# Kernel tuning notes

Hardware: AMD Instinct MI355X
Metric: run time of the kernel (lower is better)

The kernel has to match this reference:

```python
import jax, jax.numpy as jnp
import numpy as np


def setup_inputs() -> dict:
    key = jax.random.key(0)
    ks = jax.random.split(key, 8)
    N, NL, C, E, P3, P2, P1 = 2048, 16, 128, 10, 23, 4, 1
    return {
        "x": jax.random.normal(ks[0], (N, NL, C), dtype=jnp.float32),
        "atom_types": jax.random.randint(ks[1], (N,), 0, E),
        "U3": jax.random.normal(ks[2], (NL, NL, NL, P3), dtype=jnp.float32),
        "U2": jax.random.normal(ks[3], (NL, NL, P2), dtype=jnp.float32),
        "U1": jax.random.normal(ks[4], (NL, P1), dtype=jnp.float32),
        "W3": jax.random.normal(ks[5], (E, P3, C), dtype=jnp.float32),
        "W2": jax.random.normal(ks[6], (E, P2, C), dtype=jnp.float32),
        "W1": jax.random.normal(ks[7], (E, P1, C), dtype=jnp.float32),
    }


def reference(x, atom_types, U3, U2, U1, W3, W2, W1):
    # MACE symmetric contraction, correlation order 3, per-atom-type weights.
    # x: [N, nl, C]; atom_types: [N]; U3: [nl,nl,nl,P3]; W3: [E,P3,C]; etc.
    w3 = W3[atom_types]  # [N, P3, C]
    w2 = W2[atom_types]  # [N, P2, C]
    w1 = W1[atom_types]  # [N, P1, C]
    # Correlation-3 term: c3[n,a,b,c] = sum_{i,k} U3[a,b,i,k] * w3[n,k,c] * x[n,i,c]
    xw = jnp.einsum('nkc,nic->nkic', w3, x)        # [N, P3, nl, C]
    c3 = jnp.einsum('abik,nkic->nabc', U3, xw)     # [N, nl, nl, C]
    # Add correlation-2 term, contract one nl index with x.
    c2 = c3 + jnp.einsum('abk,nkc->nabc', U2, w2)  # [N, nl, nl, C]
    c1 = jnp.einsum('nabc,nbc->nac', c2, x)        # [N, nl, C]
    # Add correlation-1 term, contract last nl index with x.
    c1 = c1 + jnp.einsum('ak,nkc->nac', U1, w1)    # [N, nl, C]
    out = jnp.einsum('nac,nac->nc', c1, x)         # [N, C]
    return out
```

## Files before the change

kernel.cpp:

```cpp
#include <hip/hip_runtime.h>


constexpr int NL = 16;
constexpr int CC = 128;
constexpr int EE = 10;
constexpr int P3 = 23;
constexpr int P2 = 4;
constexpr int P1 = 1;
constexpr int NTRI = 816;
constexpr int NPAIR = 136;
constexpr int GG = 4;
constexpr int S1 = 4;
constexpr int S2 = 8;

constexpr int pairsBefore(int a) {
    int s = 0;
    for (int x = 0; x < a; x++) s += NL - x;
    return s;
}
constexpr int trisBefore(int a) {
    int s = 0;
    for (int x = 0; x < a; x++) s += (NL - x) * (NL - x + 1) / 2;
    return s;
}
static_assert(trisBefore(S1) % 4 == 0, "tri split1 must be float4-aligned");
static_assert(pairsBefore(S1) % 2 == 0, "pair split1 must be float2-aligned");
static_assert(trisBefore(S2) % 4 == 0, "tri split2 must be float4-aligned");
static_assert(pairsBefore(S2) % 2 == 0, "pair split2 must be float2-aligned");

__global__ void k_pre(const float* __restrict__ U3, const float* __restrict__ U2,
                      const float* __restrict__ U1,
                      const float* __restrict__ W3, const float* __restrict__ W2,
                      const float* __restrict__ W1,
                      const int* __restrict__ types,
                      float* __restrict__ A3, float* __restrict__ A2,
                      float* __restrict__ A1,
                      int* __restrict__ buckets, int* __restrict__ groups,
                      int* __restrict__ ngroups, int N) {
    constexpr int NB3 = EE * (NTRI / 4);
    constexpr int NB2 = EE * (NPAIR / 2);
    __shared__ float u3l[4 * P3];
    __shared__ float u2l[2 * P2];
    __shared__ int scnt[EE];
    __shared__ int goff[EE + 1];
    int b = blockIdx.x;
    int tid = threadIdx.x;

    if (b < NB3) {
        int t = b / (NTRI / 4), tri4 = b % (NTRI / 4);
        for (int idx = tid; idx < 4 * P3; idx += blockDim.x) {
            int lt = idx / P3, k = idx % P3;
            int tri = tri4 * 4 + lt;
            int rem = tri, a = 0;
            while (rem >= (NL - a) * (NL - a + 1) / 2) { rem -= (NL - a) * (NL - a + 1) / 2; a++; }
            int bb = a;
            while (rem >= NL - bb) { rem -= NL - bb; bb++; }
            int i = bb + rem;
            auto u = [&](int p, int q, int r) { return U3[((p * NL + q) * NL + r) * P3 + k]; };
            float s = u(a,bb,i) + u(a,i,bb) + u(bb,a,i) + u(bb,i,a) + u(i,a,bb) + u(i,bb,a);
            int m = (a == bb && bb == i) ? 6 : ((a == bb || bb == i) ? 2 : 1);
            u3l[idx] = s / (float)m;
        }
        __syncthreads();
        int c = tid;
        float4 sv = {0.f, 0.f, 0.f, 0.f};
        #pragma unroll
        for (int k = 0; k < P3; k++) {
            float w = W3[(t * P3 + k) * CC + c];
            sv.x += u3l[0 * P3 + k] * w;
            sv.y += u3l[1 * P3 + k] * w;
            sv.z += u3l[2 * P3 + k] * w;
            sv.w += u3l[3 * P3 + k] * w;
        }
        ((float4*)A3)[((size_t)t * (NTRI / 4) + tri4) * CC + c] = sv;
    } else if (b < NB3 + NB2) {
        int j = b - NB3;
        int t = j / (NPAIR / 2), pr2 = j % (NPAIR / 2);
        for (int idx = tid; idx < 2 * P2; idx += blockDim.x) {
            int lp = idx / P2, k = idx % P2;
            int pr = pr2 * 2 + lp;
            int rem = pr, a = 0;
            while (rem >= NL - a) { rem -= NL - a; a++; }
            int bb = a + rem;
            float s = U2[(a * NL + bb) * P2 + k];
            if (a != bb) s += U2[(bb * NL + a) * P2 + k];
            u2l[idx] = s;
        }
        __syncthreads();
        int c = tid;
        float2 sv = {0.f, 0.f};
        #pragma unroll
        for (int k = 0; k < P2; k++) {
            float w = W2[(t * P2 + k) * CC + c];
            sv.x += u2l[0 * P2 + k] * w;
            sv.y += u2l[1 * P2 + k] * w;
        }
        ((float2*)A2)[((size_t)t * (NPAIR / 2) + pr2) * CC + c] = sv;
    } else if (b < NB3 + NB2 + EE) {
        int t = b - NB3 - NB2;
        int c = tid;
        #pragma unroll
        for (int a = 0; a < NL; a++) {
            A1[((size_t)t * NL + a) * CC + c] = U1[a * P1] * W1[(size_t)t * P1 * CC + c];
        }
    } else {
        if (tid < EE) scnt[tid] = 0;
        __syncthreads();
        for (int n = tid; n < N; n += blockDim.x) {
            int t = types[n];
            int pos = atomicAdd(&scnt[t], 1);
            buckets[t * N + pos] = n;
        }
        __syncthreads();
        if (tid == 0) {
            int off = 0;
            for (int t = 0; t < EE; t++) { goff[t] = off; off += (scnt[t] + GG - 1) / GG; }
            goff[EE] = off;
            *ngroups = off;
        }
        __syncthreads();
        for (int t = 0; t < EE; t++) {
            int cnt = scnt[t];
            int ng = (cnt + GG - 1) / GG;
            for (int g = tid; g < ng; g += blockDim.x) {
                int* gr = &groups[(goff[t] + g) * 8];
                int nv = cnt - g * GG; if (nv > GG) nv = GG;
                gr[0] = t;
                gr[5] = nv;
                for (int j = 0; j < GG; j++) {
                    int jj = j < nv ? j : nv - 1;
                    gr[1 + j] = buckets[t * N + g * GG + jj];
                }
            }
        }
    }
}

template <int A0, int A1, bool LIN>
__device__ __forceinline__ void eval_nest(const float (&xv)[GG][NL],
                                          const float4* __restrict__ a3v,
                                          const float2* __restrict__ a2v,
                                          const float* __restrict__ a1p,
                                          float (&acc)[GG]) {
    if (LIN) {
        #pragma unroll
        for (int a = 0; a < NL; a++) {
            float w = a1p[a * CC];
            #pragma unroll
            for (int g = 0; g < GG; g++) acc[g] += w * xv[g][a];
        }
    }
    float4 w4 = {0.f, 0.f, 0.f, 0.f};
    float2 wp = {0.f, 0.f};
    int tri = trisBefore(A0), pr = pairsBefore(A0);
    #pragma unroll
    for (int a = A0; a < A1; a++) {
        #pragma unroll
        for (int b = a; b < NL; b++) {
            float p[GG];
            #pragma unroll
            for (int g = 0; g < GG; g++) p[g] = xv[g][a] * xv[g][b];
            if ((pr & 1) == 0) wp = a2v[(size_t)(pr >> 1) * CC];
            float w2 = ((pr & 1) == 0) ? wp.x : wp.y;
            pr++;
            #pragma unroll
            for (int g = 0; g < GG; g++) acc[g] += w2 * p[g];
            #pragma unroll
            for (int i = b; i < NL; i++) {
                if ((tri & 3) == 0) w4 = a3v[(size_t)(tri >> 2) * CC];
                int r = tri & 3;
                float w3 = (r == 0) ? w4.x : (r == 1) ? w4.y : (r == 2) ? w4.z : w4.w;
                tri++;
                #pragma unroll
                for (int g = 0; g < GG; g++) acc[g] += w3 * (p[g] * xv[g][i]);
            }
        }
    }
}

__global__ __launch_bounds__(CC, 3) void k_main(const float* __restrict__ x,
                                                const float* __restrict__ A3,
                                                const float* __restrict__ A2,
                                                const float* __restrict__ A1,
                                                const int* __restrict__ groups,
                                                const int* __restrict__ ngroups,
                                                float* __restrict__ out) {
    int pb = blockIdx.x;
    int nb = gridDim.x;
    int q = nb >> 3, r = nb & 7;
    int xcd = pb & 7, sub = pb >> 3;
    int blk = (xcd < r ? xcd * (q + 1) : r * (q + 1) + (xcd - r) * q) + sub;
    if (blk >= *ngroups) return;
    const int* gr = groups + blk * 8;
    int t = gr[0];
    int nvalid = gr[5];
    int c = threadIdx.x;

    int na[GG];
    #pragma unroll
    for (int g = 0; g < GG; g++) na[g] = gr[1 + g];

    float xv[GG][NL];
    #pragma unroll
    for (int g = 0; g < GG; g++)
        #pragma unroll
        for (int i = 0; i < NL; i++)
            xv[g][i] = x[((size_t)na[g] * NL + i) * CC + c];

    const float4* a3v = (const float4*)A3 + (size_t)t * (NTRI / 4) * CC + c;
    const float2* a2v = (const float2*)A2 + (size_t)t * (NPAIR / 2) * CC + c;
    const float* a1p = A1 + (size_t)t * NL * CC + c;

    float acc[GG] = {0.f, 0.f, 0.f, 0.f};
    if (blockIdx.y == 0)
        eval_nest<0, S1, true>(xv, a3v, a2v, a1p, acc);
    else if (blockIdx.y == 1)
        eval_nest<S1, S2, false>(xv, a3v, a2v, a1p, acc);
    else
        eval_nest<S2, NL, false>(xv, a3v, a2v, a1p, acc);

    #pragma unroll
    for (int g = 0; g < GG; g++)
        if (g < nvalid) atomicAdd(&out[(size_t)na[g] * CC + c], acc[g]);
}

extern "C" void kernel_launch(void* const* d_in, const int* in_sizes, int n_in,
                              void* d_out, int out_size, void* d_ws, size_t ws_size,
                              hipStream_t stream) {
    const float* x   = (const float*)d_in[0];
    const int* types = (const int*)d_in[1];
    const float* U3  = (const float*)d_in[2];
    const float* U2  = (const float*)d_in[3];
    const float* U1  = (const float*)d_in[4];
    const float* W3  = (const float*)d_in[5];
    const float* W2  = (const float*)d_in[6];
    const float* W1  = (const float*)d_in[7];
    float* out = (float*)d_out;
    int N = in_sizes[1];

    int ngmax = (N + GG - 1) / GG + EE;

    float* ws   = (float*)d_ws;
    float* A3   = ws;
    float* A2   = A3 + (size_t)EE * NTRI * CC;
    float* A1   = A2 + (size_t)EE * NPAIR * CC;
    int* buckets = (int*)(A1 + (size_t)EE * NL * CC);
    int* groups  = buckets + (size_t)EE * N;
    int* ngroups = groups + (size_t)ngmax * 8;

    hipMemsetAsync(out, 0, (size_t)out_size * sizeof(float), stream);

    constexpr int NB3 = EE * (NTRI / 4);
    constexpr int NB2 = EE * (NPAIR / 2);
    hipLaunchKernelGGL(k_pre, dim3(NB3 + NB2 + EE + 1), dim3(CC), 0, stream,
                       U3, U2, U1, W3, W2, W1, types,
                       A3, A2, A1, buckets, groups, ngroups, N);
    hipLaunchKernelGGL(k_main, dim3(ngmax, 3), dim3(CC), 0, stream,
                       x, A3, A2, A1, groups, ngroups, out);
}
```

Before: 108.7 us.

## Split main kernel into four a-slices, load partial x, batch precompute blocks

The main kernel now splits the outer 'a' loop into four slices (0-2, 2-4, 4-8, 8-16) instead of three. Each slice loads only the x rows it needs, which lowers register pressure and evens out the triangular work across blocks. The pair weights are now read as scalars so splits no longer need float2 alignment. The precompute kernel handles 16 triangles or 8 pairs per block instead of 4 or 2, cutting its block count. In exchange there are more atomicAdds to out and more blocks in the main grid.

```diff
diff --git a/kernel.cpp b/kernel.cpp
--- a/kernel.cpp
+++ b/kernel.cpp
@@ -10,8 +10,9 @@
 constexpr int NTRI = 816;
 constexpr int NPAIR = 136;
 constexpr int GG = 4;
-constexpr int S1 = 4;
-constexpr int S2 = 8;
+constexpr int S1 = 2;
+constexpr int S2 = 4;
+constexpr int S3 = 8;
 
 constexpr int pairsBefore(int a) {
     int s = 0;
@@ -24,9 +25,8 @@
     return s;
 }
 static_assert(trisBefore(S1) % 4 == 0, "tri split1 must be float4-aligned");
-static_assert(pairsBefore(S1) % 2 == 0, "pair split1 must be float2-aligned");
 static_assert(trisBefore(S2) % 4 == 0, "tri split2 must be float4-aligned");
-static_assert(pairsBefore(S2) % 2 == 0, "pair split2 must be float2-aligned");
+static_assert(trisBefore(S3) % 4 == 0, "tri split3 must be float4-aligned");
 
 __global__ void k_pre(const float* __restrict__ U3, const float* __restrict__ U2,
                       const float* __restrict__ U1,
@@ -37,20 +37,22 @@
                       float* __restrict__ A1,
                       int* __restrict__ buckets, int* __restrict__ groups,
                       int* __restrict__ ngroups, int N) {
-    constexpr int NB3 = EE * (NTRI / 4);
-    constexpr int NB2 = EE * (NPAIR / 2);
-    __shared__ float u3l[4 * P3];
-    __shared__ float u2l[2 * P2];
+    constexpr int TB = 16;
+    constexpr int PB = 8;
+    constexpr int NB3 = EE * (NTRI / TB);
+    constexpr int NB2 = EE * (NPAIR / PB);
+    __shared__ float u3l[TB * P3];
+    __shared__ float u2l[PB * P2];
     __shared__ int scnt[EE];
     __shared__ int goff[EE + 1];
     int b = blockIdx.x;
     int tid = threadIdx.x;
 
     if (b < NB3) {
-        int t = b / (NTRI / 4), tri4 = b % (NTRI / 4);
-        for (int idx = tid; idx < 4 * P3; idx += blockDim.x) {
+        int t = b / (NTRI / TB), tri16 = b % (NTRI / TB);
+        for (int idx = tid; idx < TB * P3; idx += blockDim.x) {
             int lt = idx / P3, k = idx % P3;
-            int tri = tri4 * 4 + lt;
+            int tri = tri16 * TB + lt;
             int rem = tri, a = 0;
             while (rem >= (NL - a) * (NL - a + 1) / 2) { rem -= (NL - a) * (NL - a + 1) / 2; a++; }
             int bb = a;
@@ -63,22 +65,29 @@
         }
         __syncthreads();
         int c = tid;
-        float4 sv = {0.f, 0.f, 0.f, 0.f};
+        float4 sv[TB / 4];
+        #pragma unroll
+        for (int j = 0; j < TB / 4; j++) sv[j] = {0.f, 0.f, 0.f, 0.f};
         #pragma unroll
         for (int k = 0; k < P3; k++) {
             float w = W3[(t * P3 + k) * CC + c];
-            sv.x += u3l[0 * P3 + k] * w;
-            sv.y += u3l[1 * P3 + k] * w;
-            sv.z += u3l[2 * P3 + k] * w;
-            sv.w += u3l[3 * P3 + k] * w;
-        }
-        ((float4*)A3)[((size_t)t * (NTRI / 4) + tri4) * CC + c] = sv;
+            #pragma unroll
+            for (int j = 0; j < TB / 4; j++) {
+                sv[j].x += u3l[(j * 4 + 0) * P3 + k] * w;
+                sv[j].y += u3l[(j * 4 + 1) * P3 + k] * w;
+                sv[j].z += u3l[(j * 4 + 2) * P3 + k] * w;
+                sv[j].w += u3l[(j * 4 + 3) * P3 + k] * w;
+            }
+        }
+        #pragma unroll
+        for (int j = 0; j < TB / 4; j++)
+            ((float4*)A3)[((size_t)t * (NTRI / 4) + tri16 * (TB / 4) + j) * CC + c] = sv[j];
     } else if (b < NB3 + NB2) {
         int j = b - NB3;
-        int t = j / (NPAIR / 2), pr2 = j % (NPAIR / 2);
-        for (int idx = tid; idx < 2 * P2; idx += blockDim.x) {
+        int t = j / (NPAIR / PB), pr8 = j % (NPAIR / PB);
+        for (int idx = tid; idx < PB * P2; idx += blockDim.x) {
             int lp = idx / P2, k = idx % P2;
-            int pr = pr2 * 2 + lp;
+            int pr = pr8 * PB + lp;
             int rem = pr, a = 0;
             while (rem >= NL - a) { rem -= NL - a; a++; }
             int bb = a + rem;
@@ -88,14 +97,18 @@
         }
         __syncthreads();
         int c = tid;
-        float2 sv = {0.f, 0.f};
+        float s[PB];
+        #pragma unroll
+        for (int jj = 0; jj < PB; jj++) s[jj] = 0.f;
         #pragma unroll
         for (int k = 0; k < P2; k++) {
             float w = W2[(t * P2 + k) * CC + c];
-            sv.x += u2l[0 * P2 + k] * w;
-            sv.y += u2l[1 * P2 + k] * w;
-        }
-        ((float2*)A2)[((size_t)t * (NPAIR / 2) + pr2) * CC + c] = sv;
+            #pragma unroll
+            for (int jj = 0; jj < PB; jj++) s[jj] += u2l[jj * P2 + k] * w;
+        }
+        #pragma unroll
+        for (int jj = 0; jj < PB; jj++)
+            A2[((size_t)t * NPAIR + pr8 * PB + jj) * CC + c] = s[jj];
     } else if (b < NB3 + NB2 + EE) {
         int t = b - NB3 - NB2;
         int c = tid;
@@ -136,32 +149,31 @@
     }
 }
 
-template <int A0, int A1, bool LIN>
-__device__ __forceinline__ void eval_nest(const float (&xv)[GG][NL],
+template <int A0, int A1e, bool LIN>
+__device__ __forceinline__ void eval_nest(const float (&xv)[GG][NL - A0],
                                           const float4* __restrict__ a3v,
-                                          const float2* __restrict__ a2v,
+                                          const float* __restrict__ a2p,
                                           const float* __restrict__ a1p,
                                           float (&acc)[GG]) {
     if (LIN) {
+        static_assert(!LIN || A0 == 0, "linear term needs full x range");
         #pragma unroll
         for (int a = 0; a < NL; a++) {
             float w = a1p[a * CC];
             #pragma unroll
-            for (int g = 0; g < GG; g++) acc[g] += w * xv[g][a];
+            for (int g = 0; g < GG; g++) acc[g] += w * xv[g][a - A0];
         }
     }
     float4 w4 = {0.f, 0.f, 0.f, 0.f};
-    float2 wp = {0.f, 0.f};
     int tri = trisBefore(A0), pr = pairsBefore(A0);
     #pragma unroll
-    for (int a = A0; a < A1; a++) {
+    for (int a = A0; a < A1e; a++) {
         #pragma unroll
         for (int b = a; b < NL; b++) {
             float p[GG];
             #pragma unroll
-            for (int g = 0; g < GG; g++) p[g] = xv[g][a] * xv[g][b];
-            if ((pr & 1) == 0) wp = a2v[(size_t)(pr >> 1) * CC];
-            float w2 = ((pr & 1) == 0) ? wp.x : wp.y;
+            for (int g = 0; g < GG; g++) p[g] = xv[g][a - A0] * xv[g][b - A0];
+            float w2 = a2p[(size_t)pr * CC];
             pr++;
             #pragma unroll
             for (int g = 0; g < GG; g++) acc[g] += w2 * p[g];
@@ -172,10 +184,32 @@
                 float w3 = (r == 0) ? w4.x : (r == 1) ? w4.y : (r == 2) ? w4.z : w4.w;
                 tri++;
                 #pragma unroll
-                for (int g = 0; g < GG; g++) acc[g] += w3 * (p[g] * xv[g][i]);
+                for (int g = 0; g < GG; g++) acc[g] += w3 * (p[g] * xv[g][i - A0]);
             }
         }
     }
+}
+
+template <int A0, int A1e, bool LIN>
+__device__ __forceinline__ void run_slice(const float* __restrict__ x,
+                                          const float4* __restrict__ a3v,
+                                          const float* __restrict__ a2p,
+                                          const float* __restrict__ a1p,
+                                          const int (&na)[GG], int nvalid, int c,
+                                          float* __restrict__ out) {
+    float xv[GG][NL - A0];
+    #pragma unroll
+    for (int g = 0; g < GG; g++)
+        #pragma unroll
+        for (int i = A0; i < NL; i++)
+            xv[g][i - A0] = x[((size_t)na[g] * NL + i) * CC + c];
+
+    float acc[GG] = {0.f, 0.f, 0.f, 0.f};
+    eval_nest<A0, A1e, LIN>(xv, a3v, a2p, a1p, acc);
+
+    #pragma unroll
+    for (int g = 0; g < GG; g++)
+        if (g < nvalid) atomicAdd(&out[(size_t)na[g] * CC + c], acc[g]);
 }
 
 __global__ __launch_bounds__(CC, 3) void k_main(const float* __restrict__ x,
@@ -200,28 +234,18 @@
     #pragma unroll
     for (int g = 0; g < GG; g++) na[g] = gr[1 + g];
 
-    float xv[GG][NL];
-    #pragma unroll
-    for (int g = 0; g < GG; g++)
-        #pragma unroll
-        for (int i = 0; i < NL; i++)
-            xv[g][i] = x[((size_t)na[g] * NL + i) * CC + c];
-
     const float4* a3v = (const float4*)A3 + (size_t)t * (NTRI / 4) * CC + c;
-    const float2* a2v = (const float2*)A2 + (size_t)t * (NPAIR / 2) * CC + c;
+    const float* a2p = A2 + (size_t)t * NPAIR * CC + c;
     const float* a1p = A1 + (size_t)t * NL * CC + c;
 
-    float acc[GG] = {0.f, 0.f, 0.f, 0.f};
     if (blockIdx.y == 0)
-        eval_nest<0, S1, true>(xv, a3v, a2v, a1p, acc);
+        run_slice<0, S1, true>(x, a3v, a2p, a1p, na, nvalid, c, out);
     else if (blockIdx.y == 1)
-        eval_nest<S1, S2, false>(xv, a3v, a2v, a1p, acc);
+        run_slice<S1, S2, false>(x, a3v, a2p, a1p, na, nvalid, c, out);
+    else if (blockIdx.y == 2)
+        run_slice<S2, S3, false>(x, a3v, a2p, a1p, na, nvalid, c, out);
     else
-        eval_nest<S2, NL, false>(xv, a3v, a2v, a1p, acc);
-
-    #pragma unroll
-    for (int g = 0; g < GG; g++)
-        if (g < nvalid) atomicAdd(&out[(size_t)na[g] * CC + c], acc[g]);
+        run_slice<S3, NL, false>(x, a3v, a2p, a1p, na, nvalid, c, out);
 }
 
 extern "C" void kernel_launch(void* const* d_in, const int* in_sizes, int n_in,
@@ -250,11 +274,11 @@
 
     hipMemsetAsync(out, 0, (size_t)out_size * sizeof(float), stream);
 
-    constexpr int NB3 = EE * (NTRI / 4);
-    constexpr int NB2 = EE * (NPAIR / 2);
+    constexpr int NB3 = EE * (NTRI / 16);
+    constexpr int NB2 = EE * (NPAIR / 8);
     hipLaunchKernelGGL(k_pre, dim3(NB3 + NB2 + EE + 1), dim3(CC), 0, stream,
                        U3, U2, U1, W3, W2, W1, types,
                        A3, A2, A1, buckets, groups, ngroups, N);
-    hipLaunchKernelGGL(k_main, dim3(ngmax, 3), dim3(CC), 0, stream,
+    hipLaunchKernelGGL(k_main, dim3(ngmax, 4), dim3(CC), 0, stream,
                        x, A3, A2, A1, groups, ngroups, out);
 }
```

New measurement: 263.2 us. 2.42x slower.
